# Performance work log

Measured on AMD Instinct MI355X. Metric: run time of the kernel, lower is better.

## Reference

```python
import jax, jax.numpy as jnp
import numpy as np

S, B, D = 2048, 2, 2048      # seq, batch, hidden  (x is [S, B, D])
H, KV, HD = 16, 4, 128        # n_head, n_kv_head, head_dim
N_REP = H // KV               # GQA repeat factor
THETA = 10000.0


def setup_inputs() -> dict:
    key = jax.random.key(0)
    ks = jax.random.split(key, 5)
    sc = 1.0 / np.sqrt(D)
    x = jax.random.normal(ks[0], (S, B, D), jnp.float32)
    Wq = jax.random.normal(ks[1], (D, H * HD), jnp.float32) * sc
    Wk = jax.random.normal(ks[2], (D, KV * HD), jnp.float32) * sc
    Wv = jax.random.normal(ks[3], (D, KV * HD), jnp.float32) * sc
    Wo = jax.random.normal(ks[4], (H * HD, D), jnp.float32) * sc
    return {"x": x, "Wq": Wq, "Wk": Wk, "Wv": Wv, "Wo": Wo}


def _rope_cos_sin(seq_len, dim, theta):
    inv_freq = 1.0 / (theta ** (jnp.arange(0, dim, 2, dtype=jnp.float32) / dim))
    t = jnp.arange(seq_len, dtype=jnp.float32)
    freqs = jnp.outer(t, inv_freq)                  # [S, dim/2]
    emb = jnp.concatenate([freqs, freqs], axis=-1)  # [S, dim]
    return jnp.cos(emb), jnp.sin(emb)


def _rotate_half(u):
    u1, u2 = jnp.split(u, 2, axis=-1)
    return jnp.concatenate([-u2, u1], axis=-1)


def reference(x, Wq, Wk, Wv, Wo):
    # projections (torch Linear without bias; W stored as [in, out] here)
    q = (x @ Wq).reshape(S, B, H, HD)
    k = (x @ Wk).reshape(S, B, KV, HD)
    v = (x @ Wv).reshape(S, B, KV, HD)

    # RoPE (full rotary, partial_rotary_factor == 1.0)
    cos, sin = _rope_cos_sin(S, HD, THETA)
    cos = cos[:, None, None, :]  # [S,1,1,HD] broadcasts over B, heads
    sin = sin[:, None, None, :]
    q = q * cos + _rotate_half(q) * sin
    k = k * cos + _rotate_half(k) * sin

    # GQA: repeat_interleave kv heads to match query heads
    k = jnp.repeat(k, N_REP, axis=2)
    v = jnp.repeat(v, N_REP, axis=2)

    # [S,B,H,HD] -> [B,H,S,HD]
    q = q.transpose(1, 2, 0, 3)
    k = k.transpose(1, 2, 0, 3)
    v = v.transpose(1, 2, 0, 3)

    # causal SDPA (dropout_p = 0 in eval)
    scale = 1.0 / np.sqrt(HD)
    scores = jnp.einsum('bhqd,bhkd->bhqk', q, k) * scale
    causal = jnp.tril(jnp.ones((S, S), dtype=bool))
    scores = jnp.where(causal, scores, jnp.finfo(scores.dtype).min)
    probs = jax.nn.softmax(scores, axis=-1)
    out = jnp.einsum('bhqk,bhkd->bhqd', probs, v)

    # [B,H,S,HD] -> [S,B,D], then output projection
    out = out.transpose(2, 0, 1, 3).reshape(S, B, D)
    return out @ Wo
```

## Files before the change

### kernel.cpp

```cpp
#include <hip/hip_runtime.h>
#include <hip/hip_bf16.h>
#include <cstdint>
#include <math.h>

#define S_LEN   2048
#define B_SZ    2
#define D_MODEL 2048
#define NH      16
#define NKV     4
#define HD      128
#define ROWS    (S_LEN * B_SZ)
#define NQKV    3072
#define SCALE   0.08838834764831845f
#define QSCALE  (0.08838834764831845f * 1.4426950408889634f)
#define CBIAS   16.0f

typedef __attribute__((ext_vector_type(8))) short short8;
typedef __attribute__((ext_vector_type(4))) float f32x4;

__device__ __forceinline__ short f2bf(float f) {
  union { float f; unsigned u; } v; v.f = f;
  unsigned r = v.u + 0x7fffu + ((v.u >> 16) & 1u);
  return (short)(r >> 16);
}
__device__ __forceinline__ float bf2f(short x) {
  union { unsigned u; float f; } v;
  v.u = ((unsigned)(unsigned short)x) << 16;
  return v.f;
}
__device__ __forceinline__ float fast_exp2(float x) {
  float r; asm("v_exp_f32 %0, %1" : "=v"(r) : "v"(x)); return r;
}

__device__ __forceinline__ void async16(const short* g, short* l) {
  __builtin_amdgcn_global_load_lds(
      (const __attribute__((address_space(1))) void*)(uintptr_t)(const void*)g,
      (__attribute__((address_space(3))) void*)(uintptr_t)(void*)l,
      16, 0, 0);
}

template<int N> __device__ __forceinline__ void vm_wait() {
  asm volatile("s_waitcnt vmcnt(%0)" :: "n"(N) : "memory");
}

__host__ __device__ constexpr int sw_steady(int p, int ACALLS, int CALLS, int ISS) {
  int a = ACALLS - p - 2; if (a < 0) a = 0;
  int b = (p + 1) * ISS;  if (b > CALLS) b = CALLS;
  return a + b;
}
__host__ __device__ constexpr int sw_last(int p, int ACALLS) {
  int a = ACALLS - p - 2; return a < 0 ? 0 : a;
}

__global__ __launch_bounds__(256) void prep_kernel(
    const float* __restrict__ x,  const float* __restrict__ Wq,
    const float* __restrict__ Wk, const float* __restrict__ Wv,
    const float* __restrict__ Wo, short* __restrict__ xb,
    short* __restrict__ Wqkv_t,   short* __restrict__ Wo_t) {
  __shared__ float tile[32][33];
  const int bidx = blockIdx.x, tid = threadIdx.x;
  const int tx = tid & 31, ty = tid >> 5;
  if (bidx < 8192) {
    const int t = bidx * 256 + tid;
    float4 v = ((const float4*)x)[t];
    short4 o;
    o.x = f2bf(v.x); o.y = f2bf(v.y); o.z = f2bf(v.z); o.w = f2bf(v.w);
    *(short4*)(xb + (size_t)t * 4) = o;
  } else if (bidx < 14336) {
    const int idx = bidx - 8192;
    const int bx = idx % 96, k0 = (idx / 96) * 32;
    const float* src; int Ndim, n0, drow;
    if (bx < 64)      { src = Wq; Ndim = 2048; n0 = bx * 32;        drow = n0; }
    else if (bx < 80) { src = Wk; Ndim = 512;  n0 = (bx - 64) * 32; drow = 2048 + n0; }
    else              { src = Wv; Ndim = 512;  n0 = (bx - 80) * 32; drow = 2560 + n0; }
    for (int r = ty; r < 32; r += 8)
      tile[r][tx] = src[(size_t)(k0 + r) * Ndim + n0 + tx];
    __syncthreads();
    for (int r = ty; r < 32; r += 8)
      Wqkv_t[(size_t)(drow + r) * 2048 + k0 + tx] = f2bf(tile[tx][r]);
  } else {
    const int idx = bidx - 14336;
    const int n0 = (idx & 63) * 32, k0 = (idx >> 6) * 32;
    for (int r = ty; r < 32; r += 8)
      tile[r][tx] = Wo[(size_t)(k0 + r) * 2048 + n0 + tx];
    __syncthreads();
    for (int r = ty; r < 32; r += 8)
      Wo_t[(size_t)(n0 + r) * 2048 + k0 + tx] = f2bf(tile[tx][r]);
  }
}

template<int BM, int BN, int BF16OUT, int MINW>
__global__ __launch_bounds__(512, MINW) void gemm3_kernel(const short* __restrict__ A,
    const short* __restrict__ Bt, void* __restrict__ Cv, int N, int K) {
  constexpr int MGRP  = BM / 16;
  constexpr int MI    = BM / 32;
  constexpr int NP    = MI / 2;
  constexpr int NGRP  = BN / 16;
  constexpr int NJ    = BN / 64;
  constexpr int BCALLS = NGRP / 4;
  constexpr int ACALLS = MGRP / 4;
  constexpr int CALLS = BCALLS + ACALLS;
  constexpr int ISS   = (NP == 4) ? 2 : 3;
  constexpr int BS_SH = NGRP * 1024;
  constexpr int BUFSH = BS_SH + MGRP * 1024;
  __shared__ alignas(16) short lds[2 * BUFSH];

  const int tid  = threadIdx.x;
  const int w    = tid >> 6, lane = tid & 63;
  const int quad = lane >> 4, lr = lane & 15;
  const int wm   = w >> 2, wn = w & 3;

  const int nwg = gridDim.x;
  const int id  = (blockIdx.x & 7) * (nwg >> 3) + (blockIdx.x >> 3);
  const int nbx = N / BN;
  const int bx = id % nbx, by = id / nbx;
  const int m0 = by * BM, n0 = bx * BN;

  const short* gsrc[CALLS];
  int dsts[CALLS];
#pragma unroll
  for (int c = 0; c < CALLS; ++c) {
    if (c < BCALLS) {
      const int sb = c * 8 + w, ng = sb >> 1, kk = sb & 1;
      gsrc[c] = Bt + (size_t)(n0 + ng * 16 + lr) * K + kk * 32 + quad * 8;
      dsts[c] = sb * 512;
    } else {
      const int p = c - BCALLS;
      const int mg = (w >> 2) * (MGRP / 2) + 2 * p + ((w >> 1) & 1), kk = w & 1;
      gsrc[c] = A + (size_t)(m0 + mg * 16 + lr) * K + kk * 32 + quad * 8;
      dsts[c] = BS_SH + (p * 8 + w) * 512;
    }
  }

  f32x4 acc[MI][NJ];
#pragma unroll
  for (int i = 0; i < MI; ++i)
#pragma unroll
    for (int j = 0; j < NJ; ++j) acc[i][j] = (f32x4){0.f, 0.f, 0.f, 0.f};

  auto stage = [&](int t, int c) {
    async16(gsrc[c] + (size_t)t * 64, lds + (t & 1) * BUFSH + dsts[c]);
  };

  const int NT = K >> 6;
#pragma unroll
  for (int c = 0; c < CALLS; ++c) stage(0, c);
  vm_wait<ACALLS - 1>();
  __builtin_amdgcn_s_barrier();
  asm volatile("" ::: "memory");

  for (int t = 0; t < NT; ++t) {
    const short* lb = lds + (t & 1) * BUFSH;
    const bool pre = (t + 1) < NT;
    short8 b[NJ][2];
#pragma unroll
    for (int p = 0; p < NP; ++p) {
      if (p == 0) {
#pragma unroll
        for (int j = 0; j < NJ; ++j)
#pragma unroll
          for (int kk = 0; kk < 2; ++kk)
            b[j][kk] = *(const short8*)(lb + ((wn * NJ + j) * 2 + kk) * 512 + lane * 8);
      }
      short8 a[2][2];
#pragma unroll
      for (int e = 0; e < 2; ++e)
#pragma unroll
        for (int kk = 0; kk < 2; ++kk)
          a[e][kk] = *(const short8*)(lb + BS_SH + (p * 8 + (wm * 2 + e) * 2 + kk) * 512 + lane * 8);
      if (pre) {
#pragma unroll
        for (int c = p * ISS; c < ((p + 1) * ISS < CALLS ? (p + 1) * ISS : CALLS); ++c)
          stage(t + 1, c);
      }
      asm volatile("" ::: "memory");
      __builtin_amdgcn_s_barrier();
      asm volatile("s_waitcnt lgkmcnt(0)" ::: "memory");
      __builtin_amdgcn_s_setprio(1);
#pragma unroll
      for (int kk = 0; kk < 2; ++kk)
#pragma unroll
        for (int e = 0; e < 2; ++e)
#pragma unroll
          for (int j = 0; j < NJ; ++j)
            acc[2 * p + e][j] = __builtin_amdgcn_mfma_f32_16x16x32_bf16(a[e][kk], b[j][kk], acc[2 * p + e][j], 0, 0, 0);
      __builtin_amdgcn_s_setprio(0);
      if (pre) {
        if (p == NP - 1)      vm_wait<ACALLS - 1>();
        else if (p == 0)      vm_wait<sw_steady(0, ACALLS, CALLS, ISS)>();
        else if (p == 1)      vm_wait<sw_steady(1, ACALLS, CALLS, ISS)>();
        else if (p == 2)      vm_wait<sw_steady(2, ACALLS, CALLS, ISS)>();
      } else {
        if (p == 0 && NP > 1)      vm_wait<sw_last(0, ACALLS)>();
        else if (p == 1 && NP > 2) vm_wait<sw_last(1, ACALLS)>();
        else if (p == 2 && NP > 3) vm_wait<sw_last(2, ACALLS)>();
      }
      asm volatile("" ::: "memory");
      __builtin_amdgcn_s_barrier();
      asm volatile("" ::: "memory");
    }
  }

#pragma unroll
  for (int i = 0; i < MI; ++i) {
    const int row = m0 + wm * (BM / 2) + i * 16 + quad * 4;
#pragma unroll
    for (int j = 0; j < NJ; ++j) {
      const int col = n0 + wn * (16 * NJ) + j * 16 + lr;
#pragma unroll
      for (int r = 0; r < 4; ++r) {
        const float v = acc[i][j][r];
        if (BF16OUT) ((short*)Cv)[(size_t)(row + r) * N + col] = f2bf(v);
        else         ((float*)Cv)[(size_t)(row + r) * N + col] = v;
      }
    }
  }
}

__global__ __launch_bounds__(256) void ropevpack_kernel(
    const short* __restrict__ QKVb, short* __restrict__ Qb,
    short* __restrict__ Kpack, short* __restrict__ Vpack) {
  __shared__ short vtile[32][136];
  const int bidx = blockIdx.x, tid = threadIdx.x;
  if (bidx < 20480) {
    const int head = bidx >> 10;
    const int t = (bidx & 1023) * 256 + tid;
    const int i = t & 63;
    const int row = t >> 6;
    const int s = row >> 1;
    const int b = row & 1;
    float inv_freq = __expf(-(float)i * (1.0f / 64.0f) * 9.210340371976184f);
    float ang = (float)s * inv_freq;
    float sn, cs;
    __sincosf(ang, &sn, &cs);
    if (head < NH) {
      const short* p = QKVb + (size_t)row * NQKV + head * HD;
      float v1 = bf2f(p[i]), v2 = bf2f(p[i + 64]);
      short* q = Qb + ((size_t)(b * NH + head) * S_LEN + s) * HD;
      q[i]      = f2bf((v1 * cs - v2 * sn) * QSCALE);
      q[i + 64] = f2bf((v2 * cs + v1 * sn) * QSCALE);
    } else {
      const int kv = head - NH;
      const short* p = QKVb + (size_t)row * NQKV + NH * HD + kv * HD;
      float v1 = bf2f(p[i]), v2 = bf2f(p[i + 64]);
      float k1 = v1 * cs - v2 * sn;
      float k2 = v2 * cs + v1 * sn;
      short* kp = Kpack + (size_t)(b * NKV + kv) * S_LEN * HD;
      const int tile = s >> 4, lrr = s & 15;
      const int d1 = i, d2 = i + 64;
      kp[(size_t)((tile * 4 + (d1 >> 5)) * 64 + ((d1 >> 3) & 3) * 16 + lrr) * 8 + (d1 & 7)] = f2bf(k1);
      kp[(size_t)((tile * 4 + (d2 >> 5)) * 64 + ((d2 >> 3) & 3) * 16 + lrr) * 8 + (d2 & 7)] = f2bf(k2);
    }
  } else {
    const int vb = bidx - 20480;
    const int chunk = vb & 63, stream = vb >> 6;
    const int b = stream >> 2, kv = stream & 3;
    const int vcol = NH * HD + NKV * HD + kv * HD;
    {
      const int r = tid >> 3, c = (tid & 7) * 16;
      const short* src = QKVb + (size_t)((chunk * 32 + r) * B_SZ + b) * NQKV + vcol + c;
      *(short8*)(&vtile[r][c])     = *(const short8*)(src);
      *(short8*)(&vtile[r][c + 8]) = *(const short8*)(src + 8);
    }
    __syncthreads();
    const int wave = tid >> 6, lane = tid & 63, quad = lane >> 4, lr = lane & 15;
    short* dst = Vpack + (size_t)stream * HD * S_LEN + chunk * 4096 + lane * 8;
#pragma unroll
    for (int k = 0; k < 2; ++k) {
      const int dt = wave + k * 4;
      short8 v;
#pragma unroll
      for (int j = 0; j < 8; ++j) v[j] = vtile[quad * 8 + j][dt * 16 + lr];
      *(short8*)(dst + dt * 512) = v;
    }
  }
}

#define PSP 72

template<bool MASK>
__device__ __forceinline__ void attn_iter64(
    const short* __restrict__ Ks, const short* __restrict__ Vs,
    short* __restrict__ Psw, const short8 qf[4], int kv0, int nt, int qlim,
    int quad, int lr, int lane, f32x4 o[8], float& l_i)
{
  const int lane_off = lane * 8;
  f32x4 sc[4];
#pragma unroll
  for (int t = 0; t < 4; ++t) {
    if (t < nt) {
      const short* kp = Ks + t * 2048 + lane_off;
      f32x4 s = (f32x4){-CBIAS, -CBIAS, -CBIAS, -CBIAS};
#pragma unroll
      for (int c = 0; c < 4; ++c) {
        short8 kf = *(const short8*)(kp + c * 512);
        s = __builtin_amdgcn_mfma_f32_16x16x32_bf16(kf, qf[c], s, 0, 0, 0);
      }
      sc[t] = s;
    } else {
      sc[t] = (f32x4){-3.0e38f, -3.0e38f, -3.0e38f, -3.0e38f};
    }
  }
  if (MASK) {
#pragma unroll
    for (int t = 0; t < 4; ++t)
#pragma unroll
      for (int r = 0; r < 4; ++r)
        if (kv0 + t * 16 + quad * 4 + r > qlim) sc[t][r] = -3.0e38f;
  }
  float rs = 0.f;
#pragma unroll
  for (int t = 0; t < 4; ++t) {
    float p0 = fast_exp2(sc[t][0]);
    float p1 = fast_exp2(sc[t][1]);
    float p2 = fast_exp2(sc[t][2]);
    float p3 = fast_exp2(sc[t][3]);
    rs += (p0 + p1) + (p2 + p3);
    __hip_bfloat162 pk01 = __float22bfloat162_rn(make_float2(p0, p1));
    __hip_bfloat162 pk23 = __float22bfloat162_rn(make_float2(p2, p3));
    union { __hip_bfloat162 h2[2]; uint2 u; } pu;
    pu.h2[0] = pk01; pu.h2[1] = pk23;
    *(uint2*)(Psw + lr * PSP + t * 16 + quad * 4) = pu.u;
  }
  rs += __shfl_xor(rs, 16, 64);
  rs += __shfl_xor(rs, 32, 64);
  l_i += rs;
  short8 pb0 = *(const short8*)(Psw + lr * PSP + quad * 8);
#pragma unroll
  for (int dt = 0; dt < 8; ++dt) {
    short8 vf = *(const short8*)(Vs + dt * 512 + lane_off);
    o[dt] = __builtin_amdgcn_mfma_f32_16x16x32_bf16(vf, pb0, o[dt], 0, 0, 0);
  }
  if (!MASK || nt > 2) {
    short8 pb1 = *(const short8*)(Psw + lr * PSP + 32 + quad * 8);
#pragma unroll
    for (int dt = 0; dt < 8; ++dt) {
      short8 vf = *(const short8*)(Vs + 4096 + dt * 512 + lane_off);
      o[dt] = __builtin_amdgcn_mfma_f32_16x16x32_bf16(vf, pb1, o[dt], 0, 0, 0);
    }
  }
}

__global__ __launch_bounds__(256) void attn_kernel(const short* __restrict__ Qb,
    const short* __restrict__ Kpack, const short* __restrict__ Vpack,
    short* __restrict__ Ob) {
  __shared__ alignas(16) short Ks[64 * HD];
  __shared__ alignas(16) short Vs[64 * HD];
  __shared__ alignas(16) short Ps[4][16 * PSP];
  const int tid = threadIdx.x, wave = tid >> 6, lane = tid & 63;
  const int quad = lane >> 4, lr = lane & 15;
  const int bid = blockIdx.x;
  const int sid  = bid & 7;
  const int hsub = (bid >> 3) & 3;
  const int qg   = 31 - (bid >> 5);
  const int b = sid >> 2, kvh = sid & 3;
  const int h = kvh * 4 + hsub;
  const int qw = (qg * 4 + wave) * 16;

  const short* Qp  = Qb    + ((size_t)(b * NH + h) * S_LEN + qw) * HD;
  const short* Kpk = Kpack + (size_t)(b * NKV + kvh) * S_LEN * HD;
  const short* Vpk = Vpack + (size_t)(b * NKV + kvh) * HD * S_LEN;
  short* Psw = &Ps[wave][0];

  short8 qf[4];
#pragma unroll
  for (int c = 0; c < 4; ++c)
    qf[c] = *(const short8*)(Qp + lr * HD + c * 32 + quad * 8);

  f32x4 o[8];
#pragma unroll
  for (int n = 0; n < 8; ++n) o[n] = (f32x4){0.f, 0.f, 0.f, 0.f};
  float l_i = 0.f;

  const int qlim = qw + lr;
  for (int it = 0; it <= qg; ++it) {
    const int kv0 = it * 64;
    __syncthreads();
    {
      const short* gk = Kpk + (size_t)kv0 * HD;
      const short* gv = Vpk + (size_t)(kv0 >> 5) * 4096;
#pragma unroll
      for (int k = 0; k < 4; ++k) {
        const int off = (wave * 4 + k) * 512;
        async16(gk + off + lane * 8, Ks + off);
        async16(gv + off + lane * 8, Vs + off);
      }
    }
    __syncthreads();
    if (it < qg)
      attn_iter64<false>(Ks, Vs, Psw, qf, kv0, 4, qlim, quad, lr, lane, o, l_i);
    else
      attn_iter64<true>(Ks, Vs, Psw, qf, kv0, wave + 1, qlim, quad, lr, lane, o, l_i);
  }

  const float invl = 1.0f / l_i;
  short* op = Ob + ((size_t)(qw + lr) * B_SZ + b) * D_MODEL + h * HD + quad * 4;
#pragma unroll
  for (int dt = 0; dt < 8; ++dt) {
    short4 ov;
    ov.x = f2bf(o[dt][0] * invl);
    ov.y = f2bf(o[dt][1] * invl);
    ov.z = f2bf(o[dt][2] * invl);
    ov.w = f2bf(o[dt][3] * invl);
    *(short4*)(op + dt * 16) = ov;
  }
}

extern "C" void kernel_launch(void* const* d_in, const int* in_sizes, int n_in,
                              void* d_out, int out_size, void* d_ws, size_t ws_size,
                              hipStream_t stream) {
  (void)in_sizes; (void)n_in; (void)out_size; (void)ws_size;
  const float* x  = (const float*)d_in[0];
  const float* Wq = (const float*)d_in[1];
  const float* Wk = (const float*)d_in[2];
  const float* Wv = (const float*)d_in[3];
  const float* Wo = (const float*)d_in[4];
  float* out = (float*)d_out;
  char* ws = (char*)d_ws;

  short* Wqkv_t = (short*)(ws);
  short* xb     = (short*)(ws + 12582912);
  short* Qb     = (short*)(ws);
  short* Kpack  = (short*)(ws + 16777216);
  short* Vpack  = (short*)(ws + 25165824);
  short* QKVb   = (short*)(ws + 29360128);
  short* Ob     = (short*)(ws + 29360128);
  short* Wo_t   = (short*)(ws + 54525952);

  prep_kernel<<<dim3(18432), 256, 0, stream>>>(x, Wq, Wk, Wv, Wo, xb, Wqkv_t, Wo_t);
  gemm3_kernel<256, 192, 1, 2><<<dim3((NQKV / 192) * (ROWS / 256)), 512, 0, stream>>>(xb, Wqkv_t, QKVb, NQKV, D_MODEL);
  ropevpack_kernel<<<dim3(20992), 256, 0, stream>>>(QKVb, Qb, Kpack, Vpack);
  attn_kernel<<<dim3(1024), 256, 0, stream>>>(Qb, Kpack, Vpack, Ob);
  gemm3_kernel<128, 128, 0, 4><<<dim3((D_MODEL / 128) * (ROWS / 128)), 512, 0, stream>>>(Ob, Wo_t, out, D_MODEL, D_MODEL);
}
```

Before: 309.3 us.

## Add double-buffered async-copy GEMM for QKV projection and retile output GEMM

Adds a new gemm4 kernel that loads A and B tiles into two LDS buffers with async 16-byte global-to-LDS copies. The next K-tile is staged while MFMA runs on the current one, with one barrier per iteration, raised wave priority around the MFMA block, and an XCD-aware block remap. The QKV projection now uses this kernel. Separately, the output projection GEMM is retiled from 128x128 to 128x256 with a different template parameter. The aim is to hide global load latency and cut synchronisation, at the cost of a larger LDS footprint that may limit occupancy.

New measurement: 319.8 us. +3.4%, slower.

```diff
diff --git a/kernel.cpp b/kernel.cpp
--- a/kernel.cpp
+++ b/kernel.cpp
@@ -217,6 +217,112 @@
   }
 }
 
+template<int BM, int BN, int BF16OUT>
+__global__ __launch_bounds__(512, 2) void gemm4_kernel(const short* __restrict__ A,
+    const short* __restrict__ Bt, void* __restrict__ Cv, int N, int K) {
+  constexpr int MGRP  = BM / 16;
+  constexpr int MI    = BM / 32;
+  constexpr int NP    = MI / 2;
+  constexpr int NGRP  = BN / 16;
+  constexpr int NJ    = BN / 64;
+  constexpr int BCALLS = NGRP / 4;
+  constexpr int ACALLS = MGRP / 4;
+  constexpr int CALLS = BCALLS + ACALLS;
+  constexpr int BS_SH = NGRP * 1024;
+  constexpr int BUFSH = BS_SH + MGRP * 1024;
+  __shared__ alignas(16) short lds[2 * BUFSH];
+
+  const int tid  = threadIdx.x;
+  const int w    = tid >> 6, lane = tid & 63;
+  const int quad = lane >> 4, lr = lane & 15;
+  const int wm   = w >> 2, wn = w & 3;
+
+  const int nwg = gridDim.x;
+  const int id  = (blockIdx.x & 7) * (nwg >> 3) + (blockIdx.x >> 3);
+  const int nbx = N / BN;
+  const int bx = id % nbx, by = id / nbx;
+  const int m0 = by * BM, n0 = bx * BN;
+
+  const short* gsrc[CALLS];
+  int dsts[CALLS];
+#pragma unroll
+  for (int c = 0; c < CALLS; ++c) {
+    if (c < BCALLS) {
+      const int sb = c * 8 + w, ng = sb >> 1, kk = sb & 1;
+      gsrc[c] = Bt + (size_t)(n0 + ng * 16 + lr) * K + kk * 32 + quad * 8;
+      dsts[c] = sb * 512;
+    } else {
+      const int p = c - BCALLS;
+      const int mg = (w >> 2) * (MGRP / 2) + 2 * p + ((w >> 1) & 1), kk = w & 1;
+      gsrc[c] = A + (size_t)(m0 + mg * 16 + lr) * K + kk * 32 + quad * 8;
+      dsts[c] = BS_SH + (p * 8 + w) * 512;
+    }
+  }
+
+  f32x4 acc[MI][NJ];
+#pragma unroll
+  for (int i = 0; i < MI; ++i)
+#pragma unroll
+    for (int j = 0; j < NJ; ++j) acc[i][j] = (f32x4){0.f, 0.f, 0.f, 0.f};
+
+  auto stage = [&](int t, int c) {
+    async16(gsrc[c] + (size_t)t * 64, lds + (t & 1) * BUFSH + dsts[c]);
+  };
+
+  const int NT = K >> 6;
+#pragma unroll
+  for (int c = 0; c < CALLS; ++c) stage(0, c);
+  __syncthreads();
+
+  for (int t = 0; t < NT; ++t) {
+    const short* lb = lds + (t & 1) * BUFSH;
+    if (t + 1 < NT) {
+#pragma unroll
+      for (int c = 0; c < CALLS; ++c) stage(t + 1, c);
+    }
+    short8 b[NJ][2];
+#pragma unroll
+    for (int j = 0; j < NJ; ++j)
+#pragma unroll
+      for (int kk = 0; kk < 2; ++kk)
+        b[j][kk] = *(const short8*)(lb + ((wn * NJ + j) * 2 + kk) * 512 + lane * 8);
+#pragma unroll
+    for (int p = 0; p < NP; ++p) {
+      short8 a[2][2];
+#pragma unroll
+      for (int e = 0; e < 2; ++e)
+#pragma unroll
+        for (int kk = 0; kk < 2; ++kk)
+          a[e][kk] = *(const short8*)(lb + BS_SH + (p * 8 + (wm * 2 + e) * 2 + kk) * 512 + lane * 8);
+      __builtin_amdgcn_s_setprio(1);
+#pragma unroll
+      for (int kk = 0; kk < 2; ++kk)
+#pragma unroll
+        for (int e = 0; e < 2; ++e)
+#pragma unroll
+          for (int j = 0; j < NJ; ++j)
+            acc[2 * p + e][j] = __builtin_amdgcn_mfma_f32_16x16x32_bf16(a[e][kk], b[j][kk], acc[2 * p + e][j], 0, 0, 0);
+      __builtin_amdgcn_s_setprio(0);
+    }
+    __syncthreads();
+  }
+
+#pragma unroll
+  for (int i = 0; i < MI; ++i) {
+    const int row = m0 + wm * (BM / 2) + i * 16 + quad * 4;
+#pragma unroll
+    for (int j = 0; j < NJ; ++j) {
+      const int col = n0 + wn * (16 * NJ) + j * 16 + lr;
+#pragma unroll
+      for (int r = 0; r < 4; ++r) {
+        const float v = acc[i][j][r];
+        if (BF16OUT) ((short*)Cv)[(size_t)(row + r) * N + col] = f2bf(v);
+        else         ((float*)Cv)[(size_t)(row + r) * N + col] = v;
+      }
+    }
+  }
+}
+
 __global__ __launch_bounds__(256) void ropevpack_kernel(
     const short* __restrict__ QKVb, short* __restrict__ Qb,
     short* __restrict__ Kpack, short* __restrict__ Vpack) {
@@ -428,8 +534,8 @@
   short* Wo_t   = (short*)(ws + 54525952);
 
   prep_kernel<<<dim3(18432), 256, 0, stream>>>(x, Wq, Wk, Wv, Wo, xb, Wqkv_t, Wo_t);
-  gemm3_kernel<256, 192, 1, 2><<<dim3((NQKV / 192) * (ROWS / 256)), 512, 0, stream>>>(xb, Wqkv_t, QKVb, NQKV, D_MODEL);
+  gemm4_kernel<256, 192, 1><<<dim3((NQKV / 192) * (ROWS / 256)), 512, 0, stream>>>(xb, Wqkv_t, QKVb, NQKV, D_MODEL);
   ropevpack_kernel<<<dim3(20992), 256, 0, stream>>>(QKVb, Qb, Kpack, Vpack);
   attn_kernel<<<dim3(1024), 256, 0, stream>>>(Qb, Kpack, Vpack, Ob);
-  gemm3_kernel<128, 128, 0, 4><<<dim3((D_MODEL / 128) * (ROWS / 128)), 512, 0, stream>>>(Ob, Wo_t, out, D_MODEL, D_MODEL);
-}
+  gemm3_kernel<128, 256, 0, 2><<<dim3((D_MODEL / 256) * (ROWS / 128)), 512, 0, stream>>>(Ob, Wo_t, out, D_MODEL, D_MODEL);
+}
```
